# Kernel optimization log

Measured on AMD Instinct MI355X. Metric: run time of the kernel, lower is better.

Reference implementation:

```python
import jax, jax.numpy as jnp
import numpy as np

B, L, D = 8, 4096, 768
EPS = 1e-5


def layer_norm(x, g, b):
    mu = jnp.mean(x, axis=-1, keepdims=True)
    var = jnp.mean(jnp.square(x - mu), axis=-1, keepdims=True)
    return (x - mu) * jax.lax.rsqrt(var + EPS) * g + b


def conv1d_same(x_blc, w_oik, b_o):
    # x_blc: [B, L, C] -> torch Conv1d(C, C, 3, padding=1) on [B, C, L]
    x_ncw = jnp.swapaxes(x_blc, 1, 2)
    y = jax.lax.conv_general_dilated(
        x_ncw, w_oik, window_strides=(1,), padding=[(1, 1)],
        dimension_numbers=("NCW", "OIW", "NCW"))
    y = y + b_o[None, :, None]
    return jnp.swapaxes(y, 1, 2)


def simple_ssm(u, a_p, b_p, c_p, d_p):
    # Diagonal SSM: h_t = sigmoid(a)*h_{t-1} + b*u_t ; y_t = c*h_t + d*u_t
    a = jax.nn.sigmoid(a_p)  # [D]

    def step(h, ut):  # h, ut: [B, D]
        h = a * h + b_p * ut
        return h, c_p * h

    h0 = jnp.zeros((u.shape[0], u.shape[2]), u.dtype)
    _, y = jax.lax.scan(step, h0, jnp.swapaxes(u, 0, 1))  # y: [L, B, D]
    return jnp.swapaxes(y, 0, 1) + d_p * u


def setup_inputs() -> dict:
    key = jax.random.key(0)
    ks = jax.random.split(key, 16)
    s_lin = 1.0 / np.sqrt(D)
    s_conv = 1.0 / np.sqrt(3 * D)
    return {
        "x": jax.random.normal(ks[0], (B, L, D), jnp.float32),
        "ln_g": jnp.ones((D,), jnp.float32),
        "ln_b": jnp.zeros((D,), jnp.float32),
        "Wi": jax.random.normal(ks[1], (D, 2 * D), jnp.float32) * s_lin,
        "bi": jnp.zeros((2 * D,), jnp.float32),
        "Wf_conv": jax.random.normal(ks[2], (D, D, 3), jnp.float32) * s_conv,
        "bf_conv": jnp.zeros((D,), jnp.float32),
        "af": jax.random.normal(ks[3], (D,), jnp.float32),
        "bf": jax.random.normal(ks[4], (D,), jnp.float32) * 0.5,
        "cf": jax.random.normal(ks[5], (D,), jnp.float32) * 0.5,
        "df": jax.random.normal(ks[6], (D,), jnp.float32) * 0.5,
        "Wb_conv": jax.random.normal(ks[7], (D, D, 3), jnp.float32) * s_conv,
        "bb_conv": jnp.zeros((D,), jnp.float32),
        "ab": jax.random.normal(ks[8], (D,), jnp.float32),
        "bb": jax.random.normal(ks[9], (D,), jnp.float32) * 0.5,
        "cb": jax.random.normal(ks[10], (D,), jnp.float32) * 0.5,
        "db": jax.random.normal(ks[11], (D,), jnp.float32) * 0.5,
        "Wo": jax.random.normal(ks[12], (D, D), jnp.float32) * s_lin,
        "bo": jnp.zeros((D,), jnp.float32),
    }


def reference(x, ln_g, ln_b, Wi, bi, Wf_conv, bf_conv, af, bf, cf, df,
              Wb_conv, bb_conv, ab, bb, cb, db, Wo, bo):
    residual = x
    xn = layer_norm(x, ln_g, ln_b)
    proj = xn @ Wi + bi                      # [B, L, 2D]
    xg, z = proj[..., :D], proj[..., D:]
    # forward branch
    f = conv1d_same(xg, Wf_conv, bf_conv)
    f = simple_ssm(f, af, bf, cf, df)
    # backward branch (flip along sequence)
    b_in = jnp.flip(xg, axis=1)
    bb_out = conv1d_same(b_in, Wb_conv, bb_conv)
    bb_out = simple_ssm(bb_out, ab, bb, cb, db)
    bb_out = jnp.flip(bb_out, axis=1)
    zg = jax.nn.silu(z)
    y = f * zg + bb_out * zg
    return y @ Wo + bo + residual
```

## Files before the change

kernel.cpp:

```cpp
#include <hip/hip_runtime.h>
#include <cstdint>
#include <cstddef>
#include <math.h>

#define L_SEQ 4096
#define D_DIM 768
#define B_SZ 8
#define M_ROWS (B_SZ * L_SEQ)
#define CHUNK 64

typedef __bf16 bf16x8 __attribute__((ext_vector_type(8)));
typedef float floatx4 __attribute__((ext_vector_type(4)));

#define GLP(p)  ((__attribute__((address_space(1))) const void*)(const void*)(p))
#define LDSP(p) ((__attribute__((address_space(3))) void*)(void*)(p))

__global__ __launch_bounds__(256) void ln_kernel(const float* __restrict__ x,
                                                 const float* __restrict__ g,
                                                 const float* __restrict__ b,
                                                 __bf16* __restrict__ xn) {
  __shared__ float red[256];
  const int tid = threadIdx.x;
  const size_t row = blockIdx.x;
  const float* xr = x + row * D_DIM;
  float v0 = xr[tid];
  float v1 = xr[tid + 256];
  float v2 = xr[tid + 512];
  red[tid] = v0 + v1 + v2;
  __syncthreads();
  for (int off = 128; off > 0; off >>= 1) {
    if (tid < off) red[tid] += red[tid + off];
    __syncthreads();
  }
  float mu = red[0] * (1.0f / D_DIM);
  __syncthreads();
  float d0 = v0 - mu, d1 = v1 - mu, d2 = v2 - mu;
  red[tid] = d0 * d0 + d1 * d1 + d2 * d2;
  __syncthreads();
  for (int off = 128; off > 0; off >>= 1) {
    if (tid < off) red[tid] += red[tid + off];
    __syncthreads();
  }
  float rs = rsqrtf(red[0] * (1.0f / D_DIM) + 1e-5f);
  __bf16* xo = xn + row * D_DIM;
  xo[tid]       = (__bf16)(d0 * rs * g[tid]       + b[tid]);
  xo[tid + 256] = (__bf16)(d1 * rs * g[tid + 256] + b[tid + 256]);
  xo[tid + 512] = (__bf16)(d2 * rs * g[tid + 512] + b[tid + 512]);
}


#define VMW(n) asm volatile("s_waitcnt vmcnt(" #n ")" ::: "memory")
#define BARR   asm volatile("s_barrier" ::: "memory")
#define MF(a, b, c) __builtin_amdgcn_mfma_f32_16x16x32_bf16((a), (b), (c), 0, 0, 0)
#define LDV(off) (*(const bf16x8*)(smem + (off)))

#define RDA(BUF, MOFF) do { \
  aR0k0 = LDV((BUF)*65536 + aoff + (MOFF) + ck0);        aR0k1 = LDV((BUF)*65536 + aoff + (MOFF) + ck1); \
  aR1k0 = LDV((BUF)*65536 + aoff + (MOFF) + 2048 + ck0); aR1k1 = LDV((BUF)*65536 + aoff + (MOFF) + 2048 + ck1); \
  aR2k0 = LDV((BUF)*65536 + aoff + (MOFF) + 4096 + ck0); aR2k1 = LDV((BUF)*65536 + aoff + (MOFF) + 4096 + ck1); \
  aR3k0 = LDV((BUF)*65536 + aoff + (MOFF) + 6144 + ck0); aR3k1 = LDV((BUF)*65536 + aoff + (MOFF) + 6144 + ck1); \
} while (0)

#define RDB01(BUF) do { \
  bN0k0 = LDV((BUF)*65536 + boff + ck0);        bN0k1 = LDV((BUF)*65536 + boff + ck1); \
  bN1k0 = LDV((BUF)*65536 + boff + 2048 + ck0); bN1k1 = LDV((BUF)*65536 + boff + 2048 + ck1); \
} while (0)

#define RDB23(BUF) do { \
  bN2k0 = LDV((BUF)*65536 + boff + 4096 + ck0); bN2k1 = LDV((BUF)*65536 + boff + 4096 + ck1); \
  bN3k0 = LDV((BUF)*65536 + boff + 6144 + ck0); bN3k1 = LDV((BUF)*65536 + boff + 6144 + ck1); \
} while (0)

#define MMQ01(AI) do { \
  acc[(AI)+0][0] = MF(aR0k0, bN0k0, acc[(AI)+0][0]); acc[(AI)+0][0] = MF(aR0k1, bN0k1, acc[(AI)+0][0]); \
  acc[(AI)+0][1] = MF(aR0k0, bN1k0, acc[(AI)+0][1]); acc[(AI)+0][1] = MF(aR0k1, bN1k1, acc[(AI)+0][1]); \
  acc[(AI)+1][0] = MF(aR1k0, bN0k0, acc[(AI)+1][0]); acc[(AI)+1][0] = MF(aR1k1, bN0k1, acc[(AI)+1][0]); \
  acc[(AI)+1][1] = MF(aR1k0, bN1k0, acc[(AI)+1][1]); acc[(AI)+1][1] = MF(aR1k1, bN1k1, acc[(AI)+1][1]); \
  acc[(AI)+2][0] = MF(aR2k0, bN0k0, acc[(AI)+2][0]); acc[(AI)+2][0] = MF(aR2k1, bN0k1, acc[(AI)+2][0]); \
  acc[(AI)+2][1] = MF(aR2k0, bN1k0, acc[(AI)+2][1]); acc[(AI)+2][1] = MF(aR2k1, bN1k1, acc[(AI)+2][1]); \
  acc[(AI)+3][0] = MF(aR3k0, bN0k0, acc[(AI)+3][0]); acc[(AI)+3][0] = MF(aR3k1, bN0k1, acc[(AI)+3][0]); \
  acc[(AI)+3][1] = MF(aR3k0, bN1k0, acc[(AI)+3][1]); acc[(AI)+3][1] = MF(aR3k1, bN1k1, acc[(AI)+3][1]); \
} while (0)

#define MMQ23(AI) do { \
  acc[(AI)+0][2] = MF(aR0k0, bN2k0, acc[(AI)+0][2]); acc[(AI)+0][2] = MF(aR0k1, bN2k1, acc[(AI)+0][2]); \
  acc[(AI)+0][3] = MF(aR0k0, bN3k0, acc[(AI)+0][3]); acc[(AI)+0][3] = MF(aR0k1, bN3k1, acc[(AI)+0][3]); \
  acc[(AI)+1][2] = MF(aR1k0, bN2k0, acc[(AI)+1][2]); acc[(AI)+1][2] = MF(aR1k1, bN2k1, acc[(AI)+1][2]); \
  acc[(AI)+1][3] = MF(aR1k0, bN3k0, acc[(AI)+1][3]); acc[(AI)+1][3] = MF(aR1k1, bN3k1, acc[(AI)+1][3]); \
  acc[(AI)+2][2] = MF(aR2k0, bN2k0, acc[(AI)+2][2]); acc[(AI)+2][2] = MF(aR2k1, bN2k1, acc[(AI)+2][2]); \
  acc[(AI)+2][3] = MF(aR2k0, bN3k0, acc[(AI)+2][3]); acc[(AI)+2][3] = MF(aR2k1, bN3k1, acc[(AI)+2][3]); \
  acc[(AI)+3][2] = MF(aR3k0, bN2k0, acc[(AI)+3][2]); acc[(AI)+3][2] = MF(aR3k1, bN2k1, acc[(AI)+3][2]); \
  acc[(AI)+3][3] = MF(aR3k0, bN3k0, acc[(AI)+3][3]); acc[(AI)+3][3] = MF(aR3k1, bN3k1, acc[(AI)+3][3]); \
} while (0)

#define STAGE_A_HP(h, p, tkt, BUF) do { \
  const __bf16* _s; \
  if (MODE == 1) { \
    const int _kb = ((tkt) * 43) >> 9;                        \
    const int _io = (((tkt) - _kb * 12) << 6) + (_kb - 1) * D_DIM; \
    _s = ((unsigned)(lv##h##p + _kb - 1) < (unsigned)L_SEQ) ? (rb##h##p + _io) : zbuf; \
  } else { \
    _s = rb##h##p + (tkt) * 64; \
  } \
  __builtin_amdgcn_global_load_lds(GLP(_s), \
      LDSP(smem + (BUF)*65536 + (h)*8192 + (p)*16384 + dstw), 16, 0, 0); \
} while (0)

#define STAGE_B_HP(h, p, tkt, BUF) \
  __builtin_amdgcn_global_load_lds(GLP(pB##h##p + (tkt) * 64), \
      LDSP(smem + (BUF)*65536 + 32768 + (h)*16384 + (p)*8192 + dstw), 16, 0, 0)

#define TILE(T, BUF, VA, VC, SA1, SREST) do { \
   \
  VMW(VA); BARR; \
  RDB01(BUF); RDA(BUF, 0); \
  if (SA1) { STAGE_A_HP(1, 0, (T) + 1, (BUF) ^ 1); STAGE_A_HP(1, 1, (T) + 1, (BUF) ^ 1); } \
  __builtin_amdgcn_s_setprio(1); MMQ01(0); __builtin_amdgcn_s_setprio(0); \
   \
  BARR; \
  RDB23(BUF); \
  if (SREST) { STAGE_A_HP(0, 0, (T) + 2, (BUF)); STAGE_A_HP(0, 1, (T) + 2, (BUF)); } \
  __builtin_amdgcn_s_setprio(1); MMQ23(0); __builtin_amdgcn_s_setprio(0); \
   \
  VMW(VC); BARR; \
  RDA(BUF, 8192); \
  if (SREST) { STAGE_B_HP(0, 0, (T) + 2, (BUF)); STAGE_B_HP(0, 1, (T) + 2, (BUF)); } \
  __builtin_amdgcn_s_setprio(1); MMQ01(4); __builtin_amdgcn_s_setprio(0); \
   \
  if (SREST) { STAGE_B_HP(1, 0, (T) + 2, (BUF)); STAGE_B_HP(1, 1, (T) + 2, (BUF)); } \
  __builtin_amdgcn_s_setprio(1); MMQ23(4); __builtin_amdgcn_s_setprio(0); \
} while (0)

template<int MODE, int NT, int NN>
__global__ __launch_bounds__(512) void gemm256_kernel(
    const __bf16* __restrict__ A, const __bf16* __restrict__ Bt,
    const float* __restrict__ bias_lo, const float* __restrict__ bias_hi,
    const float* __restrict__ resid,
    __bf16* __restrict__ out0, __bf16* __restrict__ out1,
    float* __restrict__ outf, const __bf16* __restrict__ zbuf) {
  extern __shared__ char smem[];
  constexpr int K = NT * 64;
  constexpr int nwg = NN * (M_ROWS / 256);
  constexpr int cpx = nwg / 8;
  const int bid = blockIdx.x;
  const int wgs = (bid & 7) * cpx + (bid >> 3);
  const int tileN = wgs % NN;
  const int tileM = wgs / NN;
  const int tid  = (int)threadIdx.x;
  const int w    = tid >> 6;
  const int lane = tid & 63;
  const int l15  = lane & 15;
  const int quad = lane >> 4;
  const int wm   = w >> 2;
  const int wn   = w & 3;

  const int srow = tid >> 3;
  const int ce   = ((tid & 7) ^ (srow & 7)) << 3;
  const int dstw = w << 10;

  const int aoff = (wm * 128 + l15) * 128;
  const int boff = 32768 + (wn * 64 + l15) * 128;
  const int ck0  = (quad ^ (l15 & 7)) << 4;
  const int ck1  = ((4 | quad) ^ (l15 & 7)) << 4;

  const __bf16* pB00 = Bt + (size_t)(tileN * 256 + srow) * K + ce;
  const __bf16* pB01 = Bt + (size_t)(tileN * 256 + 64 + srow) * K + ce;
  const __bf16* pB10 = Bt + (size_t)(tileN * 256 + 128 + srow) * K + ce;
  const __bf16* pB11 = Bt + (size_t)(tileN * 256 + 192 + srow) * K + ce;

  const __bf16 *rb00, *rb01, *rb10, *rb11;
  int lv00 = 0, lv01 = 0, lv10 = 0, lv11 = 0;
  {
    const int g00 = tileM * 256 + srow;
    const int g01 = tileM * 256 + 128 + srow;
    const int g10 = tileM * 256 + 64 + srow;
    const int g11 = tileM * 256 + 192 + srow;
    if (MODE == 1) {
      rb00 = A + (size_t)g00 * D_DIM + ce; lv00 = g00 & (L_SEQ - 1);
      rb01 = A + (size_t)g01 * D_DIM + ce; lv01 = g01 & (L_SEQ - 1);
      rb10 = A + (size_t)g10 * D_DIM + ce; lv10 = g10 & (L_SEQ - 1);
      rb11 = A + (size_t)g11 * D_DIM + ce; lv11 = g11 & (L_SEQ - 1);
    } else {
      rb00 = A + (size_t)g00 * K + ce;
      rb01 = A + (size_t)g01 * K + ce;
      rb10 = A + (size_t)g10 * K + ce;
      rb11 = A + (size_t)g11 * K + ce;
    }
  }

  bf16x8 aR0k0, aR0k1, aR1k0, aR1k1, aR2k0, aR2k1, aR3k0, aR3k1;
  bf16x8 bN0k0, bN0k1, bN1k0, bN1k1, bN2k0, bN2k1, bN3k0, bN3k1;
  floatx4 acc[8][4];
#pragma unroll
  for (int i = 0; i < 8; ++i)
#pragma unroll
    for (int j = 0; j < 4; ++j)
#pragma unroll
      for (int r = 0; r < 4; ++r) acc[i][j][r] = 0.0f;

  STAGE_A_HP(0, 0, 0, 0); STAGE_A_HP(0, 1, 0, 0);
  STAGE_B_HP(0, 0, 0, 0); STAGE_B_HP(0, 1, 0, 0);
  STAGE_B_HP(1, 0, 0, 0); STAGE_B_HP(1, 1, 0, 0);
  STAGE_A_HP(1, 0, 0, 0); STAGE_A_HP(1, 1, 0, 0);
  STAGE_A_HP(0, 0, 1, 1); STAGE_A_HP(0, 1, 1, 1);
  STAGE_B_HP(0, 0, 1, 1); STAGE_B_HP(0, 1, 1, 1);
  STAGE_B_HP(1, 0, 1, 1); STAGE_B_HP(1, 1, 1, 1);

  for (int it = 0; it < (NT - 2) / 2; ++it) {
    const int T0 = it * 2;
    TILE(T0,     0, 8, 10, 1, 1);
    TILE(T0 + 1, 1, 8, 10, 1, 1);
  }
  TILE(NT - 2, 0, 8, 8, 1, 0);
  TILE(NT - 1, 1, 2, 0, 0, 0);

  const int rowb = tileM * 256 + wm * 128 + quad * 4;
  const int colb = tileN * 256 + wn * 64 + l15;
#pragma unroll
  for (int mi = 0; mi < 8; ++mi) {
#pragma unroll
    for (int nj = 0; nj < 4; ++nj) {
      const int col = colb + nj * 16;
      float bv;
      if (MODE == 3) bv = bias_lo[col];
      else bv = (col < D_DIM) ? bias_lo[col] : bias_hi[col - D_DIM];
#pragma unroll
      for (int r = 0; r < 4; ++r) {
        const int row = rowb + mi * 16 + r;
        float v = acc[mi][nj][r] + bv;
        if (MODE == 3) {
          const size_t o = (size_t)row * D_DIM + col;
          outf[o] = v + resid[o];
        } else if (MODE == 0) {
          if (col < D_DIM) out0[(size_t)row * D_DIM + col] = (__bf16)v;
          else out1[(size_t)row * D_DIM + (col - D_DIM)] = (__bf16)(v / (1.0f + expf(-v)));
        } else {
          if (col < D_DIM) out0[(size_t)row * D_DIM + col] = (__bf16)v;
          else out1[(size_t)row * D_DIM + (col - D_DIM)] = (__bf16)v;
        }
      }
    }
  }
}

__global__ __launch_bounds__(256) void scan1_kernel(
    const float* __restrict__ ap0, const float* __restrict__ bp0,
    const float* __restrict__ ap1, const float* __restrict__ bp1,
    const __bf16* __restrict__ u0, const __bf16* __restrict__ u1,
    float* __restrict__ hl) {
  int idx = blockIdx.x * 256 + threadIdx.x;
  int dg = idx % 96;
  int rest = idx / 96;
  int chunk = rest & 63;
  int tb = rest >> 6;
  int tensor = tb >> 3;
  int b = tb & 7;
  const float* ap = (tensor ? ap1 : ap0) + dg * 8;
  const float* bp = (tensor ? bp1 : bp0) + dg * 8;
  const __bf16* u = (tensor ? u1 : u0) +
      ((size_t)(b * L_SEQ + chunk * CHUNK + (tensor ? CHUNK - 1 : 0))) * D_DIM + dg * 8;
  const int st = tensor ? -D_DIM : D_DIM;
  float a[8], bb[8], h[8];
#pragma unroll
  for (int j = 0; j < 8; ++j) {
    a[j] = 1.0f / (1.0f + expf(-ap[j]));
    bb[j] = bp[j];
    h[j] = 0.0f;
  }
  for (int t = 0; t < CHUNK; ++t) {
    bf16x8 uv = *(const bf16x8*)u;
#pragma unroll
    for (int j = 0; j < 8; ++j) h[j] = a[j] * h[j] + bb[j] * (float)uv[j];
    u += st;
  }
  float* o = hl + (size_t)(tb * 64 + chunk) * D_DIM + dg * 8;
#pragma unroll
  for (int j = 0; j < 8; ++j) o[j] = h[j];
}

__global__ __launch_bounds__(256) void scan2_kernel(
    const float* __restrict__ ap0, const float* __restrict__ ap1,
    float* __restrict__ hl) {
  int idx = blockIdx.x * 256 + threadIdx.x;
  int d = idx % D_DIM;
  int tb = idx / D_DIM;
  int tensor = tb >> 3;
  const float* ap = tensor ? ap1 : ap0;
  float a = 1.0f / (1.0f + expf(-ap[d]));
  float aT = a * a;  aT *= aT;  aT *= aT;  aT *= aT;  aT *= aT;  aT *= aT;
  float* p = hl + (size_t)tb * 64 * D_DIM + d + (tensor ? 63 * D_DIM : 0);
  const int st = tensor ? -D_DIM : D_DIM;
  float carry = 0.0f;
  for (int c = 0; c < 64; ++c) {
    float tmp = *p;
    *p = carry;
    carry = aT * carry + tmp;
    p += st;
  }
}

__global__ __launch_bounds__(256) void scan3_kernel(
    const float* __restrict__ ap0, const float* __restrict__ bp0,
    const float* __restrict__ cp0, const float* __restrict__ dp0,
    const float* __restrict__ ap1, const float* __restrict__ bp1,
    const float* __restrict__ cp1, const float* __restrict__ dp1,
    __bf16* __restrict__ u0, __bf16* __restrict__ u1,
    const float* __restrict__ hl) {
  int idx = blockIdx.x * 256 + threadIdx.x;
  int dg = idx % 96;
  int rest = idx / 96;
  int chunk = rest & 63;
  int tb = rest >> 6;
  int tensor = tb >> 3;
  int b = tb & 7;
  const float* ap = (tensor ? ap1 : ap0) + dg * 8;
  const float* bp = (tensor ? bp1 : bp0) + dg * 8;
  const float* cp = (tensor ? cp1 : cp0) + dg * 8;
  const float* dp = (tensor ? dp1 : dp0) + dg * 8;
  __bf16* u = (tensor ? u1 : u0) +
      ((size_t)(b * L_SEQ + chunk * CHUNK + (tensor ? CHUNK - 1 : 0))) * D_DIM + dg * 8;
  const int st = tensor ? -D_DIM : D_DIM;
  const float* hp = hl + (size_t)(tb * 64 + chunk) * D_DIM + dg * 8;
  float a[8], bb[8], cc[8], dd[8], h[8];
#pragma unroll
  for (int j = 0; j < 8; ++j) {
    a[j] = 1.0f / (1.0f + expf(-ap[j]));
    bb[j] = bp[j]; cc[j] = cp[j]; dd[j] = dp[j];
    h[j] = hp[j];
  }
  for (int t = 0; t < CHUNK; ++t) {
    bf16x8 uv = *(const bf16x8*)u;
    bf16x8 ov;
#pragma unroll
    for (int j = 0; j < 8; ++j) {
      float xv = (float)uv[j];
      h[j] = a[j] * h[j] + bb[j] * xv;
      ov[j] = (__bf16)(cc[j] * h[j] + dd[j] * xv);
    }
    *(bf16x8*)u = ov;
    u += st;
  }
}

__global__ __launch_bounds__(256) void gate_kernel(const __bf16* __restrict__ f,
                                                   const __bf16* __restrict__ bbuf,
                                                   const __bf16* __restrict__ zg,
                                                   __bf16* __restrict__ y) {
  size_t e = ((size_t)blockIdx.x * 256 + threadIdx.x) * 8;
  bf16x8 f8 = *(const bf16x8*)(f + e);
  bf16x8 b8 = *(const bf16x8*)(bbuf + e);
  bf16x8 z8 = *(const bf16x8*)(zg + e);
  bf16x8 o;
#pragma unroll
  for (int j = 0; j < 8; ++j)
    o[j] = (__bf16)(((float)f8[j] + (float)b8[j]) * (float)z8[j]);
  *(bf16x8*)(y + e) = o;
}

__global__ __launch_bounds__(256) void tr_kernel(const float* __restrict__ in,
                                                 __bf16* __restrict__ out,
                                                 int Kdim, int Ndim) {
  int idx = blockIdx.x * 256 + threadIdx.x;
  if (idx >= Kdim * Ndim) return;
  int n = idx / Kdim;
  int k = idx - n * Kdim;
  out[idx] = (__bf16)in[(size_t)k * Ndim + n];
}

__global__ __launch_bounds__(256) void trconv_kernel(const float* __restrict__ in,
                                                     __bf16* __restrict__ out,
                                                     int rev) {
  int idx = blockIdx.x * 256 + threadIdx.x;
  if (idx >= D_DIM * 2304) return;
  int o = idx / 2304;
  int rem = idx - o * 2304;
  int k = rem / D_DIM;
  int i = rem - k * D_DIM;
  int ks = rev ? (2 - k) : k;
  out[idx] = (__bf16)in[(size_t)o * 2304 + i * 3 + ks];
}

__global__ void zero_kernel(__bf16* z) { z[threadIdx.x] = (__bf16)0.0f; }

extern "C" void kernel_launch(void* const* d_in, const int* in_sizes, int n_in,
                              void* d_out, int out_size, void* d_ws, size_t ws_size,
                              hipStream_t stream) {
  const float* x    = (const float*)d_in[0];
  const float* ln_g = (const float*)d_in[1];
  const float* ln_b = (const float*)d_in[2];
  const float* Wi   = (const float*)d_in[3];
  const float* bi   = (const float*)d_in[4];
  const float* Wf   = (const float*)d_in[5];
  const float* bfc  = (const float*)d_in[6];
  const float* af   = (const float*)d_in[7];
  const float* bfp  = (const float*)d_in[8];
  const float* cfp  = (const float*)d_in[9];
  const float* dfp  = (const float*)d_in[10];
  const float* Wb   = (const float*)d_in[11];
  const float* bbc  = (const float*)d_in[12];
  const float* ab   = (const float*)d_in[13];
  const float* bbp  = (const float*)d_in[14];
  const float* cbp  = (const float*)d_in[15];
  const float* dbp  = (const float*)d_in[16];
  const float* Wo   = (const float*)d_in[17];
  const float* bo   = (const float*)d_in[18];
  float* out = (float*)d_out;

  char* ws = (char*)d_ws;
  const size_t BLD = (size_t)B_SZ * L_SEQ * D_DIM;
  __bf16* ws0 = (__bf16*)(ws);
  __bf16* ws1 = (__bf16*)(ws + BLD * 2);
  __bf16* ws2 = (__bf16*)(ws + BLD * 4);
  __bf16* ws3 = (__bf16*)(ws + BLD * 6);
  __bf16* wit  = (__bf16*)(ws + BLD * 8);
  __bf16* wcat = wit + (size_t)1536 * 768;
  __bf16* wot  = wcat + (size_t)1536 * 2304;
  __bf16* zbuf = wot + (size_t)768 * 768;
  float* hl = (float*)(ws + BLD * 2);
  const size_t needed = BLD * 8 +
      ((size_t)1536 * 768 + (size_t)1536 * 2304 + (size_t)768 * 768) * 2 + 256;
  if (ws_size < needed) return;

  static bool attr_done = false;
  if (!attr_done) {
    (void)hipFuncSetAttribute(reinterpret_cast<const void*>(&gemm256_kernel<0, 12, 6>),
                              hipFuncAttributeMaxDynamicSharedMemorySize, 131072);
    (void)hipFuncSetAttribute(reinterpret_cast<const void*>(&gemm256_kernel<1, 36, 6>),
                              hipFuncAttributeMaxDynamicSharedMemorySize, 131072);
    (void)hipFuncSetAttribute(reinterpret_cast<const void*>(&gemm256_kernel<3, 12, 3>),
                              hipFuncAttributeMaxDynamicSharedMemorySize, 131072);
    attr_done = true;
  }

  zero_kernel<<<1, 128, 0, stream>>>(zbuf);
  tr_kernel<<<(768 * 1536 + 255) / 256, 256, 0, stream>>>(Wi, wit, 768, 1536);
  trconv_kernel<<<(768 * 2304 + 255) / 256, 256, 0, stream>>>(Wf, wcat, 0);
  trconv_kernel<<<(768 * 2304 + 255) / 256, 256, 0, stream>>>(Wb, wcat + (size_t)768 * 2304, 1);
  tr_kernel<<<(768 * 768 + 255) / 256, 256, 0, stream>>>(Wo, wot, 768, 768);

  ln_kernel<<<M_ROWS, 256, 0, stream>>>(x, ln_g, ln_b, ws0);

  gemm256_kernel<0, 12, 6><<<768, 512, 131072, stream>>>(
      ws0, wit, bi, bi + 768, nullptr, ws1, ws2, nullptr, zbuf);

  gemm256_kernel<1, 36, 6><<<768, 512, 131072, stream>>>(
      ws1, wcat, bfc, bbc, nullptr, ws0, ws3, nullptr, zbuf);

  scan1_kernel<<<384, 256, 0, stream>>>(af, bfp, ab, bbp, ws0, ws3, hl);
  scan2_kernel<<<48, 256, 0, stream>>>(af, ab, hl);
  scan3_kernel<<<384, 256, 0, stream>>>(af, bfp, cfp, dfp, ab, bbp, cbp, dbp, ws0, ws3, hl);

  gate_kernel<<<12288, 256, 0, stream>>>(ws0, ws3, ws2, ws1);

  gemm256_kernel<3, 12, 3><<<384, 512, 131072, stream>>>(
      ws1, wot, bo, bo, x, nullptr, nullptr, out, zbuf);
}
```

Measured before the change: 746.4 us.

## Restructure GEMM main loop pipeline and fuse SSM pass with gating

The GEMM main loop is rescheduled. It prefetches LDS fragments for the next tile into separate low and high A register sets, issues global-to-LDS stages in four phases separated by barriers, and waits on lgkmcnt before each MFMA group. Pointer bases are replaced with 32-bit offsets. Separately, the third scan pass is merged with the gate kernel: each thread runs the forward chunk scan and then the backward chunk scan, computing the gated output directly. This removes one full-tensor round trip, but launches only 192 blocks and adds more barriers and registers to the GEMM.

New measurement: 1.332 ms. 78.5% more time.

```diff
diff --git a/kernel.cpp b/kernel.cpp
--- a/kernel.cpp
+++ b/kernel.cpp
@@ -50,85 +50,114 @@
 
 
 #define VMW(n) asm volatile("s_waitcnt vmcnt(" #n ")" ::: "memory")
+#define LGKM0  asm volatile("s_waitcnt lgkmcnt(0)" ::: "memory")
 #define BARR   asm volatile("s_barrier" ::: "memory")
+#define SP1    __builtin_amdgcn_s_setprio(1)
+#define SP0    __builtin_amdgcn_s_setprio(0)
 #define MF(a, b, c) __builtin_amdgcn_mfma_f32_16x16x32_bf16((a), (b), (c), 0, 0, 0)
 #define LDV(off) (*(const bf16x8*)(smem + (off)))
 
-#define RDA(BUF, MOFF) do { \
-  aR0k0 = LDV((BUF)*65536 + aoff + (MOFF) + ck0);        aR0k1 = LDV((BUF)*65536 + aoff + (MOFF) + ck1); \
-  aR1k0 = LDV((BUF)*65536 + aoff + (MOFF) + 2048 + ck0); aR1k1 = LDV((BUF)*65536 + aoff + (MOFF) + 2048 + ck1); \
-  aR2k0 = LDV((BUF)*65536 + aoff + (MOFF) + 4096 + ck0); aR2k1 = LDV((BUF)*65536 + aoff + (MOFF) + 4096 + ck1); \
-  aR3k0 = LDV((BUF)*65536 + aoff + (MOFF) + 6144 + ck0); aR3k1 = LDV((BUF)*65536 + aoff + (MOFF) + 6144 + ck1); \
-} while (0)
-
-#define RDB01(BUF) do { \
-  bN0k0 = LDV((BUF)*65536 + boff + ck0);        bN0k1 = LDV((BUF)*65536 + boff + ck1); \
-  bN1k0 = LDV((BUF)*65536 + boff + 2048 + ck0); bN1k1 = LDV((BUF)*65536 + boff + 2048 + ck1); \
-} while (0)
-
-#define RDB23(BUF) do { \
-  bN2k0 = LDV((BUF)*65536 + boff + 4096 + ck0); bN2k1 = LDV((BUF)*65536 + boff + 4096 + ck1); \
-  bN3k0 = LDV((BUF)*65536 + boff + 6144 + ck0); bN3k1 = LDV((BUF)*65536 + boff + 6144 + ck1); \
-} while (0)
-
-#define MMQ01(AI) do { \
-  acc[(AI)+0][0] = MF(aR0k0, bN0k0, acc[(AI)+0][0]); acc[(AI)+0][0] = MF(aR0k1, bN0k1, acc[(AI)+0][0]); \
-  acc[(AI)+0][1] = MF(aR0k0, bN1k0, acc[(AI)+0][1]); acc[(AI)+0][1] = MF(aR0k1, bN1k1, acc[(AI)+0][1]); \
-  acc[(AI)+1][0] = MF(aR1k0, bN0k0, acc[(AI)+1][0]); acc[(AI)+1][0] = MF(aR1k1, bN0k1, acc[(AI)+1][0]); \
-  acc[(AI)+1][1] = MF(aR1k0, bN1k0, acc[(AI)+1][1]); acc[(AI)+1][1] = MF(aR1k1, bN1k1, acc[(AI)+1][1]); \
-  acc[(AI)+2][0] = MF(aR2k0, bN0k0, acc[(AI)+2][0]); acc[(AI)+2][0] = MF(aR2k1, bN0k1, acc[(AI)+2][0]); \
-  acc[(AI)+2][1] = MF(aR2k0, bN1k0, acc[(AI)+2][1]); acc[(AI)+2][1] = MF(aR2k1, bN1k1, acc[(AI)+2][1]); \
-  acc[(AI)+3][0] = MF(aR3k0, bN0k0, acc[(AI)+3][0]); acc[(AI)+3][0] = MF(aR3k1, bN0k1, acc[(AI)+3][0]); \
-  acc[(AI)+3][1] = MF(aR3k0, bN1k0, acc[(AI)+3][1]); acc[(AI)+3][1] = MF(aR3k1, bN1k1, acc[(AI)+3][1]); \
-} while (0)
-
-#define MMQ23(AI) do { \
-  acc[(AI)+0][2] = MF(aR0k0, bN2k0, acc[(AI)+0][2]); acc[(AI)+0][2] = MF(aR0k1, bN2k1, acc[(AI)+0][2]); \
-  acc[(AI)+0][3] = MF(aR0k0, bN3k0, acc[(AI)+0][3]); acc[(AI)+0][3] = MF(aR0k1, bN3k1, acc[(AI)+0][3]); \
-  acc[(AI)+1][2] = MF(aR1k0, bN2k0, acc[(AI)+1][2]); acc[(AI)+1][2] = MF(aR1k1, bN2k1, acc[(AI)+1][2]); \
-  acc[(AI)+1][3] = MF(aR1k0, bN3k0, acc[(AI)+1][3]); acc[(AI)+1][3] = MF(aR1k1, bN3k1, acc[(AI)+1][3]); \
-  acc[(AI)+2][2] = MF(aR2k0, bN2k0, acc[(AI)+2][2]); acc[(AI)+2][2] = MF(aR2k1, bN2k1, acc[(AI)+2][2]); \
-  acc[(AI)+2][3] = MF(aR2k0, bN3k0, acc[(AI)+2][3]); acc[(AI)+2][3] = MF(aR2k1, bN3k1, acc[(AI)+2][3]); \
-  acc[(AI)+3][2] = MF(aR3k0, bN2k0, acc[(AI)+3][2]); acc[(AI)+3][2] = MF(aR3k1, bN2k1, acc[(AI)+3][2]); \
-  acc[(AI)+3][3] = MF(aR3k0, bN3k0, acc[(AI)+3][3]); acc[(AI)+3][3] = MF(aR3k1, bN3k1, acc[(AI)+3][3]); \
-} while (0)
-
-#define STAGE_A_HP(h, p, tkt, BUF) do { \
-  const __bf16* _s; \
+#define RD_AL(BUF) do { \
+  aL0k0 = LDV((BUF)*65536 + aoff + ck0);        aL0k1 = LDV((BUF)*65536 + aoff + ck1); \
+  aL1k0 = LDV((BUF)*65536 + aoff + 2048 + ck0); aL1k1 = LDV((BUF)*65536 + aoff + 2048 + ck1); \
+  aL2k0 = LDV((BUF)*65536 + aoff + 4096 + ck0); aL2k1 = LDV((BUF)*65536 + aoff + 4096 + ck1); \
+  aL3k0 = LDV((BUF)*65536 + aoff + 6144 + ck0); aL3k1 = LDV((BUF)*65536 + aoff + 6144 + ck1); \
+} while (0)
+
+#define RD_AH(BUF) do { \
+  aH0k0 = LDV((BUF)*65536 + aoff + 8192 + ck0);        aH0k1 = LDV((BUF)*65536 + aoff + 8192 + ck1); \
+  aH1k0 = LDV((BUF)*65536 + aoff + 8192 + 2048 + ck0); aH1k1 = LDV((BUF)*65536 + aoff + 8192 + 2048 + ck1); \
+  aH2k0 = LDV((BUF)*65536 + aoff + 8192 + 4096 + ck0); aH2k1 = LDV((BUF)*65536 + aoff + 8192 + 4096 + ck1); \
+  aH3k0 = LDV((BUF)*65536 + aoff + 8192 + 6144 + ck0); aH3k1 = LDV((BUF)*65536 + aoff + 8192 + 6144 + ck1); \
+} while (0)
+
+#define RD_B01(BUF) do { \
+  b0k0 = LDV((BUF)*65536 + boff + ck0);        b0k1 = LDV((BUF)*65536 + boff + ck1); \
+  b1k0 = LDV((BUF)*65536 + boff + 2048 + ck0); b1k1 = LDV((BUF)*65536 + boff + 2048 + ck1); \
+} while (0)
+
+#define RD_B23(BUF) do { \
+  b2k0 = LDV((BUF)*65536 + boff + 4096 + ck0); b2k1 = LDV((BUF)*65536 + boff + 4096 + ck1); \
+  b3k0 = LDV((BUF)*65536 + boff + 6144 + ck0); b3k1 = LDV((BUF)*65536 + boff + 6144 + ck1); \
+} while (0)
+
+#define MMPA do { \
+  acc[0][0]=MF(aL0k0,b0k0,acc[0][0]); acc[0][0]=MF(aL0k1,b0k1,acc[0][0]); \
+  acc[0][1]=MF(aL0k0,b1k0,acc[0][1]); acc[0][1]=MF(aL0k1,b1k1,acc[0][1]); \
+  acc[1][0]=MF(aL1k0,b0k0,acc[1][0]); acc[1][0]=MF(aL1k1,b0k1,acc[1][0]); \
+  acc[1][1]=MF(aL1k0,b1k0,acc[1][1]); acc[1][1]=MF(aL1k1,b1k1,acc[1][1]); \
+  acc[2][0]=MF(aL2k0,b0k0,acc[2][0]); acc[2][0]=MF(aL2k1,b0k1,acc[2][0]); \
+  acc[2][1]=MF(aL2k0,b1k0,acc[2][1]); acc[2][1]=MF(aL2k1,b1k1,acc[2][1]); \
+  acc[3][0]=MF(aL3k0,b0k0,acc[3][0]); acc[3][0]=MF(aL3k1,b0k1,acc[3][0]); \
+  acc[3][1]=MF(aL3k0,b1k0,acc[3][1]); acc[3][1]=MF(aL3k1,b1k1,acc[3][1]); \
+} while (0)
+
+#define MMPB do { \
+  acc[0][2]=MF(aL0k0,b2k0,acc[0][2]); acc[0][2]=MF(aL0k1,b2k1,acc[0][2]); \
+  acc[0][3]=MF(aL0k0,b3k0,acc[0][3]); acc[0][3]=MF(aL0k1,b3k1,acc[0][3]); \
+  acc[1][2]=MF(aL1k0,b2k0,acc[1][2]); acc[1][2]=MF(aL1k1,b2k1,acc[1][2]); \
+  acc[1][3]=MF(aL1k0,b3k0,acc[1][3]); acc[1][3]=MF(aL1k1,b3k1,acc[1][3]); \
+  acc[2][2]=MF(aL2k0,b2k0,acc[2][2]); acc[2][2]=MF(aL2k1,b2k1,acc[2][2]); \
+  acc[2][3]=MF(aL2k0,b3k0,acc[2][3]); acc[2][3]=MF(aL2k1,b3k1,acc[2][3]); \
+  acc[3][2]=MF(aL3k0,b2k0,acc[3][2]); acc[3][2]=MF(aL3k1,b2k1,acc[3][2]); \
+  acc[3][3]=MF(aL3k0,b3k0,acc[3][3]); acc[3][3]=MF(aL3k1,b3k1,acc[3][3]); \
+} while (0)
+
+#define MMPC do { \
+  acc[4][0]=MF(aH0k0,b0k0,acc[4][0]); acc[4][0]=MF(aH0k1,b0k1,acc[4][0]); \
+  acc[4][1]=MF(aH0k0,b1k0,acc[4][1]); acc[4][1]=MF(aH0k1,b1k1,acc[4][1]); \
+  acc[5][0]=MF(aH1k0,b0k0,acc[5][0]); acc[5][0]=MF(aH1k1,b0k1,acc[5][0]); \
+  acc[5][1]=MF(aH1k0,b1k0,acc[5][1]); acc[5][1]=MF(aH1k1,b1k1,acc[5][1]); \
+  acc[6][0]=MF(aH2k0,b0k0,acc[6][0]); acc[6][0]=MF(aH2k1,b0k1,acc[6][0]); \
+  acc[6][1]=MF(aH2k0,b1k0,acc[6][1]); acc[6][1]=MF(aH2k1,b1k1,acc[6][1]); \
+  acc[7][0]=MF(aH3k0,b0k0,acc[7][0]); acc[7][0]=MF(aH3k1,b0k1,acc[7][0]); \
+  acc[7][1]=MF(aH3k0,b1k0,acc[7][1]); acc[7][1]=MF(aH3k1,b1k1,acc[7][1]); \
+} while (0)
+
+#define MMPD do { \
+  acc[4][2]=MF(aH0k0,b2k0,acc[4][2]); acc[4][2]=MF(aH0k1,b2k1,acc[4][2]); \
+  acc[4][3]=MF(aH0k0,b3k0,acc[4][3]); acc[4][3]=MF(aH0k1,b3k1,acc[4][3]); \
+  acc[5][2]=MF(aH1k0,b2k0,acc[5][2]); acc[5][2]=MF(aH1k1,b2k1,acc[5][2]); \
+  acc[5][3]=MF(aH1k0,b3k0,acc[5][3]); acc[5][3]=MF(aH1k1,b3k1,acc[5][3]); \
+  acc[6][2]=MF(aH2k0,b2k0,acc[6][2]); acc[6][2]=MF(aH2k1,b2k1,acc[6][2]); \
+  acc[6][3]=MF(aH2k0,b3k0,acc[6][3]); acc[6][3]=MF(aH2k1,b3k1,acc[6][3]); \
+  acc[7][2]=MF(aH3k0,b2k0,acc[7][2]); acc[7][2]=MF(aH3k1,b2k1,acc[7][2]); \
+  acc[7][3]=MF(aH3k0,b3k0,acc[7][3]); acc[7][3]=MF(aH3k1,b3k1,acc[7][3]); \
+} while (0)
+
+#define STA(h, p, tkt, BUF) do { \
+  int _off; \
   if (MODE == 1) { \
-    const int _kb = ((tkt) * 43) >> 9;                        \
+    const int _kb = ((tkt) * 43) >> 9;                  \
     const int _io = (((tkt) - _kb * 12) << 6) + (_kb - 1) * D_DIM; \
-    _s = ((unsigned)(lv##h##p + _kb - 1) < (unsigned)L_SEQ) ? (rb##h##p + _io) : zbuf; \
+    _off = ((unsigned)(lv##h##p + _kb - 1) < (unsigned)L_SEQ) ? (oa##h##p + _io) : zrel; \
   } else { \
-    _s = rb##h##p + (tkt) * 64; \
+    _off = oa##h##p + (tkt) * 64; \
   } \
-  __builtin_amdgcn_global_load_lds(GLP(_s), \
+  __builtin_amdgcn_global_load_lds(GLP(A + _off), \
       LDSP(smem + (BUF)*65536 + (h)*8192 + (p)*16384 + dstw), 16, 0, 0); \
 } while (0)
 
-#define STAGE_B_HP(h, p, tkt, BUF) \
-  __builtin_amdgcn_global_load_lds(GLP(pB##h##p + (tkt) * 64), \
+#define STB(h, p, tkt, BUF) \
+  __builtin_amdgcn_global_load_lds(GLP(Bt + ob##h##p + (tkt) * 64), \
       LDSP(smem + (BUF)*65536 + 32768 + (h)*16384 + (p)*8192 + dstw), 16, 0, 0)
 
-#define TILE(T, BUF, VA, VC, SA1, SREST) do { \
+#define TILE(T, BUF, VB, DOST, DORD) do { \
    \
-  VMW(VA); BARR; \
-  RDB01(BUF); RDA(BUF, 0); \
-  if (SA1) { STAGE_A_HP(1, 0, (T) + 1, (BUF) ^ 1); STAGE_A_HP(1, 1, (T) + 1, (BUF) ^ 1); } \
-  __builtin_amdgcn_s_setprio(1); MMQ01(0); __builtin_amdgcn_s_setprio(0); \
+  RD_AH(BUF); RD_B23(BUF); \
+  if (DOST) { STA(0, 0, (T) + 2, BUF); STA(0, 1, (T) + 2, BUF); } \
+  BARR; LGKM0; SP1; MMPA; SP0; BARR; \
    \
-  BARR; \
-  RDB23(BUF); \
-  if (SREST) { STAGE_A_HP(0, 0, (T) + 2, (BUF)); STAGE_A_HP(0, 1, (T) + 2, (BUF)); } \
-  __builtin_amdgcn_s_setprio(1); MMQ23(0); __builtin_amdgcn_s_setprio(0); \
+  if (DOST) { STA(1, 0, (T) + 2, BUF); STA(1, 1, (T) + 2, BUF); } \
+  BARR; LGKM0; SP1; MMPB; SP0; VMW(VB); BARR; \
    \
-  VMW(VC); BARR; \
-  RDA(BUF, 8192); \
-  if (SREST) { STAGE_B_HP(0, 0, (T) + 2, (BUF)); STAGE_B_HP(0, 1, (T) + 2, (BUF)); } \
-  __builtin_amdgcn_s_setprio(1); MMQ01(4); __builtin_amdgcn_s_setprio(0); \
+  if (DORD) { RD_AL((BUF) ^ 1); } \
+  if (DOST) { STB(0, 0, (T) + 2, BUF); STB(0, 1, (T) + 2, BUF); } \
+  BARR; LGKM0; SP1; MMPC; SP0; BARR; \
    \
-  if (SREST) { STAGE_B_HP(1, 0, (T) + 2, (BUF)); STAGE_B_HP(1, 1, (T) + 2, (BUF)); } \
-  __builtin_amdgcn_s_setprio(1); MMQ23(4); __builtin_amdgcn_s_setprio(0); \
+  if (DORD) { RD_B01((BUF) ^ 1); } \
+  if (DOST) { STB(1, 0, (T) + 2, BUF); STB(1, 1, (T) + 2, BUF); } \
+  BARR; LGKM0; SP1; MMPD; SP0; BARR; \
 } while (0)
 
 template<int MODE, int NT, int NN>
@@ -137,7 +166,7 @@
     const float* __restrict__ bias_lo, const float* __restrict__ bias_hi,
     const float* __restrict__ resid,
     __bf16* __restrict__ out0, __bf16* __restrict__ out1,
-    float* __restrict__ outf, const __bf16* __restrict__ zbuf) {
+    float* __restrict__ outf, int zrel) {
   extern __shared__ char smem[];
   constexpr int K = NT * 64;
   constexpr int nwg = NN * (M_ROWS / 256);
@@ -163,33 +192,31 @@
   const int ck0  = (quad ^ (l15 & 7)) << 4;
   const int ck1  = ((4 | quad) ^ (l15 & 7)) << 4;
 
-  const __bf16* pB00 = Bt + (size_t)(tileN * 256 + srow) * K + ce;
-  const __bf16* pB01 = Bt + (size_t)(tileN * 256 + 64 + srow) * K + ce;
-  const __bf16* pB10 = Bt + (size_t)(tileN * 256 + 128 + srow) * K + ce;
-  const __bf16* pB11 = Bt + (size_t)(tileN * 256 + 192 + srow) * K + ce;
-
-  const __bf16 *rb00, *rb01, *rb10, *rb11;
+  const int g00 = tileM * 256 + srow;
+  const int g10 = g00 + 64;
+  const int g01 = g00 + 128;
+  const int g11 = g00 + 192;
+  int oa00, oa01, oa10, oa11;
   int lv00 = 0, lv01 = 0, lv10 = 0, lv11 = 0;
-  {
-    const int g00 = tileM * 256 + srow;
-    const int g01 = tileM * 256 + 128 + srow;
-    const int g10 = tileM * 256 + 64 + srow;
-    const int g11 = tileM * 256 + 192 + srow;
-    if (MODE == 1) {
-      rb00 = A + (size_t)g00 * D_DIM + ce; lv00 = g00 & (L_SEQ - 1);
-      rb01 = A + (size_t)g01 * D_DIM + ce; lv01 = g01 & (L_SEQ - 1);
-      rb10 = A + (size_t)g10 * D_DIM + ce; lv10 = g10 & (L_SEQ - 1);
-      rb11 = A + (size_t)g11 * D_DIM + ce; lv11 = g11 & (L_SEQ - 1);
-    } else {
-      rb00 = A + (size_t)g00 * K + ce;
-      rb01 = A + (size_t)g01 * K + ce;
-      rb10 = A + (size_t)g10 * K + ce;
-      rb11 = A + (size_t)g11 * K + ce;
-    }
-  }
-
-  bf16x8 aR0k0, aR0k1, aR1k0, aR1k1, aR2k0, aR2k1, aR3k0, aR3k1;
-  bf16x8 bN0k0, bN0k1, bN1k0, bN1k1, bN2k0, bN2k1, bN3k0, bN3k1;
+  if (MODE == 1) {
+    oa00 = g00 * D_DIM + ce; lv00 = g00 & (L_SEQ - 1);
+    oa01 = g01 * D_DIM + ce; lv01 = g01 & (L_SEQ - 1);
+    oa10 = g10 * D_DIM + ce; lv10 = g10 & (L_SEQ - 1);
+    oa11 = g11 * D_DIM + ce; lv11 = g11 & (L_SEQ - 1);
+  } else {
+    oa00 = g00 * K + ce;
+    oa01 = g01 * K + ce;
+    oa10 = g10 * K + ce;
+    oa11 = g11 * K + ce;
+  }
+  const int ob00 = (tileN * 256 +   0 + srow) * K + ce;
+  const int ob01 = (tileN * 256 +  64 + srow) * K + ce;
+  const int ob10 = (tileN * 256 + 128 + srow) * K + ce;
+  const int ob11 = (tileN * 256 + 192 + srow) * K + ce;
+
+  bf16x8 aL0k0, aL0k1, aL1k0, aL1k1, aL2k0, aL2k1, aL3k0, aL3k1;
+  bf16x8 aH0k0, aH0k1, aH1k0, aH1k1, aH2k0, aH2k1, aH3k0, aH3k1;
+  bf16x8 b0k0, b0k1, b1k0, b1k1, b2k0, b2k1, b3k0, b3k1;
   floatx4 acc[8][4];
 #pragma unroll
   for (int i = 0; i < 8; ++i)
@@ -198,21 +225,23 @@
 #pragma unroll
       for (int r = 0; r < 4; ++r) acc[i][j][r] = 0.0f;
 
-  STAGE_A_HP(0, 0, 0, 0); STAGE_A_HP(0, 1, 0, 0);
-  STAGE_B_HP(0, 0, 0, 0); STAGE_B_HP(0, 1, 0, 0);
-  STAGE_B_HP(1, 0, 0, 0); STAGE_B_HP(1, 1, 0, 0);
-  STAGE_A_HP(1, 0, 0, 0); STAGE_A_HP(1, 1, 0, 0);
-  STAGE_A_HP(0, 0, 1, 1); STAGE_A_HP(0, 1, 1, 1);
-  STAGE_B_HP(0, 0, 1, 1); STAGE_B_HP(0, 1, 1, 1);
-  STAGE_B_HP(1, 0, 1, 1); STAGE_B_HP(1, 1, 1, 1);
-
-  for (int it = 0; it < (NT - 2) / 2; ++it) {
-    const int T0 = it * 2;
-    TILE(T0,     0, 8, 10, 1, 1);
-    TILE(T0 + 1, 1, 8, 10, 1, 1);
-  }
-  TILE(NT - 2, 0, 8, 8, 1, 0);
-  TILE(NT - 1, 1, 2, 0, 0, 0);
+  STA(0, 0, 0, 0); STA(0, 1, 0, 0); STA(1, 0, 0, 0); STA(1, 1, 0, 0);
+  STB(0, 0, 0, 0); STB(0, 1, 0, 0); STB(1, 0, 0, 0); STB(1, 1, 0, 0);
+  STA(0, 0, 1, 1); STA(0, 1, 1, 1); STA(1, 0, 1, 1); STA(1, 1, 1, 1);
+  STB(0, 0, 1, 1); STB(0, 1, 1, 1); STB(1, 0, 1, 1); STB(1, 1, 1, 1);
+  VMW(8);
+  BARR;
+  RD_AL(0); RD_B01(0);
+  LGKM0;
+  BARR;
+
+#pragma unroll 1
+  for (int T = 0; T <= NT - 4; T += 2) {
+    TILE(T,     0, 4, 1, 1);
+    TILE(T + 1, 1, 4, 1, 1);
+  }
+  TILE(NT - 2, 0, 0, 0, 1);
+  TILE(NT - 1, 1, 63, 0, 0);
 
   const int rowb = tileM * 256 + wm * 128 + quad * 4;
   const int colb = tileN * 256 + wn * 64 + l15;
@@ -299,62 +328,83 @@
   }
 }
 
-__global__ __launch_bounds__(256) void scan3_kernel(
+__global__ __launch_bounds__(256) void ssm_gate_kernel(
     const float* __restrict__ ap0, const float* __restrict__ bp0,
     const float* __restrict__ cp0, const float* __restrict__ dp0,
     const float* __restrict__ ap1, const float* __restrict__ bp1,
     const float* __restrict__ cp1, const float* __restrict__ dp1,
-    __bf16* __restrict__ u0, __bf16* __restrict__ u1,
+    __bf16* __restrict__ u0, const __bf16* __restrict__ u1,
+    const __bf16* __restrict__ zg, __bf16* __restrict__ y,
     const float* __restrict__ hl) {
   int idx = blockIdx.x * 256 + threadIdx.x;
   int dg = idx % 96;
   int rest = idx / 96;
   int chunk = rest & 63;
-  int tb = rest >> 6;
-  int tensor = tb >> 3;
-  int b = tb & 7;
-  const float* ap = (tensor ? ap1 : ap0) + dg * 8;
-  const float* bp = (tensor ? bp1 : bp0) + dg * 8;
-  const float* cp = (tensor ? cp1 : cp0) + dg * 8;
-  const float* dp = (tensor ? dp1 : dp0) + dg * 8;
-  __bf16* u = (tensor ? u1 : u0) +
-      ((size_t)(b * L_SEQ + chunk * CHUNK + (tensor ? CHUNK - 1 : 0))) * D_DIM + dg * 8;
-  const int st = tensor ? -D_DIM : D_DIM;
-  const float* hp = hl + (size_t)(tb * 64 + chunk) * D_DIM + dg * 8;
-  float a[8], bb[8], cc[8], dd[8], h[8];
-#pragma unroll
-  for (int j = 0; j < 8; ++j) {
-    a[j] = 1.0f / (1.0f + expf(-ap[j]));
-    bb[j] = bp[j]; cc[j] = cp[j]; dd[j] = dp[j];
-    h[j] = hp[j];
-  }
-  for (int t = 0; t < CHUNK; ++t) {
-    bf16x8 uv = *(const bf16x8*)u;
-    bf16x8 ov;
+  int b = rest >> 6;
+  const size_t rowbase = (size_t)(b * L_SEQ + chunk * CHUNK) * D_DIM + dg * 8;
+
+  {
+    const float* ap = ap0 + dg * 8;
+    const float* bp = bp0 + dg * 8;
+    const float* cp = cp0 + dg * 8;
+    const float* dp = dp0 + dg * 8;
+    const float* hp = hl + (size_t)(b * 64 + chunk) * D_DIM + dg * 8;
+    float a[8], bb[8], cc[8], dd[8], h[8];
 #pragma unroll
     for (int j = 0; j < 8; ++j) {
-      float xv = (float)uv[j];
-      h[j] = a[j] * h[j] + bb[j] * xv;
-      ov[j] = (__bf16)(cc[j] * h[j] + dd[j] * xv);
+      a[j] = 1.0f / (1.0f + expf(-ap[j]));
+      bb[j] = bp[j]; cc[j] = cp[j]; dd[j] = dp[j];
+      h[j] = hp[j];
     }
-    *(bf16x8*)u = ov;
-    u += st;
-  }
-}
-
-__global__ __launch_bounds__(256) void gate_kernel(const __bf16* __restrict__ f,
-                                                   const __bf16* __restrict__ bbuf,
-                                                   const __bf16* __restrict__ zg,
-                                                   __bf16* __restrict__ y) {
-  size_t e = ((size_t)blockIdx.x * 256 + threadIdx.x) * 8;
-  bf16x8 f8 = *(const bf16x8*)(f + e);
-  bf16x8 b8 = *(const bf16x8*)(bbuf + e);
-  bf16x8 z8 = *(const bf16x8*)(zg + e);
-  bf16x8 o;
-#pragma unroll
-  for (int j = 0; j < 8; ++j)
-    o[j] = (__bf16)(((float)f8[j] + (float)b8[j]) * (float)z8[j]);
-  *(bf16x8*)(y + e) = o;
+    __bf16* p = u0 + rowbase;
+    for (int t = 0; t < CHUNK; ++t) {
+      bf16x8 uv = *(const bf16x8*)p;
+      bf16x8 ov;
+#pragma unroll
+      for (int j = 0; j < 8; ++j) {
+        float xv = (float)uv[j];
+        h[j] = a[j] * h[j] + bb[j] * xv;
+        ov[j] = (__bf16)(cc[j] * h[j] + dd[j] * xv);
+      }
+      *(bf16x8*)p = ov;
+      p += D_DIM;
+    }
+  }
+
+  {
+    const float* ap = ap1 + dg * 8;
+    const float* bp = bp1 + dg * 8;
+    const float* cp = cp1 + dg * 8;
+    const float* dp = dp1 + dg * 8;
+    const float* hp = hl + (size_t)((8 + b) * 64 + chunk) * D_DIM + dg * 8;
+    float a[8], bb[8], cc[8], dd[8], h[8];
+#pragma unroll
+    for (int j = 0; j < 8; ++j) {
+      a[j] = 1.0f / (1.0f + expf(-ap[j]));
+      bb[j] = bp[j]; cc[j] = cp[j]; dd[j] = dp[j];
+      h[j] = hp[j];
+    }
+    const size_t tail = rowbase + (size_t)(CHUNK - 1) * D_DIM;
+    const __bf16* p1 = u1 + tail;
+    const __bf16* pf = u0 + tail;
+    const __bf16* pz = zg + tail;
+    __bf16* py = y + tail;
+    for (int t = 0; t < CHUNK; ++t) {
+      bf16x8 uv = *(const bf16x8*)p1;
+      bf16x8 f8 = *(const bf16x8*)pf;
+      bf16x8 z8 = *(const bf16x8*)pz;
+      bf16x8 ov;
+#pragma unroll
+      for (int j = 0; j < 8; ++j) {
+        float xv = (float)uv[j];
+        h[j] = a[j] * h[j] + bb[j] * xv;
+        float bbv = cc[j] * h[j] + dd[j] * xv;
+        ov[j] = (__bf16)(((float)f8[j] + bbv) * (float)z8[j]);
+      }
+      *(bf16x8*)py = ov;
+      p1 -= D_DIM; pf -= D_DIM; pz -= D_DIM; py -= D_DIM;
+    }
+  }
 }
 
 __global__ __launch_bounds__(256) void tr_kernel(const float* __restrict__ in,
@@ -416,7 +466,7 @@
   __bf16* wcat = wit + (size_t)1536 * 768;
   __bf16* wot  = wcat + (size_t)1536 * 2304;
   __bf16* zbuf = wot + (size_t)768 * 768;
-  float* hl = (float*)(ws + BLD * 2);
+  float* hl = (float*)wcat;
   const size_t needed = BLD * 8 +
       ((size_t)1536 * 768 + (size_t)1536 * 2304 + (size_t)768 * 768) * 2 + 256;
   if (ws_size < needed) return;
@@ -441,17 +491,16 @@
   ln_kernel<<<M_ROWS, 256, 0, stream>>>(x, ln_g, ln_b, ws0);
 
   gemm256_kernel<0, 12, 6><<<768, 512, 131072, stream>>>(
-      ws0, wit, bi, bi + 768, nullptr, ws1, ws2, nullptr, zbuf);
+      ws0, wit, bi, bi + 768, nullptr, ws1, ws2, nullptr, 0);
 
   gemm256_kernel<1, 36, 6><<<768, 512, 131072, stream>>>(
-      ws1, wcat, bfc, bbc, nullptr, ws0, ws3, nullptr, zbuf);
+      ws1, wcat, bfc, bbc, nullptr, ws0, ws3, nullptr, (int)(zbuf - ws1));
 
   scan1_kernel<<<384, 256, 0, stream>>>(af, bfp, ab, bbp, ws0, ws3, hl);
   scan2_kernel<<<48, 256, 0, stream>>>(af, ab, hl);
-  scan3_kernel<<<384, 256, 0, stream>>>(af, bfp, cfp, dfp, ab, bbp, cbp, dbp, ws0, ws3, hl);
-
-  gate_kernel<<<12288, 256, 0, stream>>>(ws0, ws3, ws2, ws1);
+  ssm_gate_kernel<<<192, 256, 0, stream>>>(af, bfp, cfp, dfp, ab, bbp, cbp, dbp,
+                                           ws0, ws3, ws2, ws1, hl);
 
   gemm256_kernel<3, 12, 3><<<384, 512, 131072, stream>>>(
-      ws1, wot, bo, bo, x, nullptr, nullptr, out, zbuf);
-}
+      ws1, wot, bo, bo, x, nullptr, nullptr, out, 0);
+}
```
